# Optimization experiments

Measured on AMD Instinct MI355X. Metric: run time of the kernel, lower is better.

Reference implementation:

```python
import jax, jax.numpy as jnp
import numpy as np

N = 100000
E = 1600000
FEAT = 128
EMB = 64
HID = 64
OUT = 16


def _glorot(key, shape):
    fan_in, fan_out = shape[1], shape[0]
    lim = (6.0 / (fan_in + fan_out)) ** 0.5
    return jax.random.uniform(key, shape, jnp.float32, -lim, lim)


def setup_inputs() -> dict:
    key = jax.random.key(0)
    ks = jax.random.split(key, 16)
    return {
        "x_feat": jax.random.normal(ks[0], (N, FEAT), jnp.float32),
        "x_emb": jax.random.normal(ks[1], (N, 2, EMB), jnp.float32),
        "edge_index": jax.random.randint(ks[2], (2, E), 0, N, jnp.int32),
        # layer 0: SAGEConv(FEAT -> HID), Linear(EMB -> HID)
        "Wl0": _glorot(ks[3], (HID, FEAT)),
        "bl0": jnp.zeros((HID,), jnp.float32),
        "Wr0": _glorot(ks[4], (HID, FEAT)),
        "We0": _glorot(ks[5], (HID, EMB)),
        "be0": jnp.zeros((HID,), jnp.float32),
        # layer 1 (last): SAGEConv(HID -> OUT), Linear(EMB==HID -> OUT)
        "Wl1": _glorot(ks[6], (OUT, HID)),
        "bl1": jnp.zeros((OUT,), jnp.float32),
        "Wr1": _glorot(ks[7], (OUT, HID)),
        "We1": _glorot(ks[8], (OUT, HID)),
        "be1": jnp.zeros((OUT,), jnp.float32),
    }


def _sage_conv(x, edge_index, Wl, bl, Wr):
    # PyG SAGEConv with mean aggregation:
    #   out = lin_l(mean_{j in N(i)} x_j) + lin_r(x_i)
    src, dst = edge_index[0], edge_index[1]
    msg = x[src]                                   # [E, C] gather
    agg = jax.ops.segment_sum(msg, dst, num_segments=N)       # [N, C]
    deg = jax.ops.segment_sum(jnp.ones((E,), x.dtype), dst, num_segments=N)
    agg = agg / jnp.maximum(deg, 1.0)[:, None]     # mean over neighbors
    return agg @ Wl.T + bl + x @ Wr.T


def reference(x_feat, x_emb, edge_index,
              Wl0, bl0, Wr0, We0, be0,
              Wl1, bl1, Wr1, We1, be1):
    # forward(x=(x_feat, x_emb), edge_index=...) path, eval mode (dropout p=0)
    e = x_emb.mean(axis=1)                         # [N, EMB]
    # layer 0 (all but last): relu(sage + linear(emb))
    h = _sage_conv(x_feat, edge_index, Wl0, bl0, Wr0)
    e = e @ We0.T + be0
    h = jax.nn.relu(h + e)
    # last layer: no relu
    h = _sage_conv(h, edge_index, Wl1, bl1, Wr1)
    e = e @ We1.T + be1
    return h + e
```

## Files before the change

kernel.cpp:

```cpp
#include <hip/hip_runtime.h>
#include <hip/hip_bf16.h>
#include <cstddef>

#define NN 100000
#define EE 1600000
#define NPB 128
#define NB  782
#define ECH 4096
#define NCH 391
#define CAP 4096

typedef __attribute__((ext_vector_type(8))) short bf16x8;
typedef __attribute__((ext_vector_type(8))) unsigned short u16x8;
typedef __attribute__((ext_vector_type(4))) float f32x4;

#define YTS 72
#define RTS 68

static inline int ceil_div(int a, int b){ return (a + b - 1) / b; }

__device__ inline unsigned short f2bf(float f){
  union { float f; unsigned u; } v; v.f = f;
  unsigned r = (v.u + 0x7fff + ((v.u >> 16) & 1)) >> 16;
  return (unsigned short)r;
}
__device__ inline float bf2f(unsigned short s){
  union { unsigned u; float f; } v; v.u = ((unsigned)s) << 16;
  return v.f;
}

#define PRE_W (128 * 192)
#define PRE_E (PRE_W + 16 * 64)
#define PRE_B (PRE_E + 16)
#define PRE_C (PRE_B + 64)
#define PRE_N (PRE_C + NB)
__global__ void prep_all_kernel(const float* __restrict__ Wl0, const float* __restrict__ Wr0,
                                const float* __restrict__ We0, const float* __restrict__ bl0,
                                const float* __restrict__ be0, const float* __restrict__ We1,
                                const float* __restrict__ be1,
                                unsigned short* __restrict__ wcat, float* __restrict__ wee,
                                float* __restrict__ b1e, float* __restrict__ bias0,
                                int* __restrict__ cur){
  int idx = blockIdx.x * blockDim.x + threadIdx.x;
  if (idx < PRE_W){
    int n = idx / 192, k = idx % 192;
    float v;
    if (n < 64) v = (k < 128) ? Wl0[n * 128 + k] : 0.f;
    else        v = (k < 128) ? Wr0[(n - 64) * 128 + k] : We0[(n - 64) * 64 + (k - 128)];
    wcat[idx] = f2bf(v);
  } else if (idx < PRE_E){
    int j = idx - PRE_W;
    int i = j >> 6, c = j & 63;
    float s = 0.f;
    for (int k = 0; k < 64; k++) s += We1[i * 64 + k] * We0[k * 64 + c];
    wee[j] = s;
  } else if (idx < PRE_B){
    int i = idx - PRE_E;
    float s = be1[i];
    for (int k = 0; k < 64; k++) s += We1[i * 64 + k] * be0[k];
    b1e[i] = s;
  } else if (idx < PRE_C){
    int i = idx - PRE_B;
    bias0[i] = bl0[i] + be0[i];
  } else if (idx < PRE_N){
    cur[idx - PRE_C] = 0;
  }
}

__global__ void eprep_kernel(const float* __restrict__ xe, unsigned short* __restrict__ eb){
  int g = blockIdx.x * blockDim.x + threadIdx.x;
  if (g >= NN * 8) return;
  int node = g >> 3, q = g & 7;
  float4 a0 = ((const float4*)xe)[(size_t)node * 32 + q * 2];
  float4 a1 = ((const float4*)xe)[(size_t)node * 32 + q * 2 + 1];
  float4 b0 = ((const float4*)xe)[(size_t)node * 32 + 16 + q * 2];
  float4 b1 = ((const float4*)xe)[(size_t)node * 32 + 16 + q * 2 + 1];
  u16x8 o;
  o[0]=f2bf(0.5f*(a0.x+b0.x)); o[1]=f2bf(0.5f*(a0.y+b0.y));
  o[2]=f2bf(0.5f*(a0.z+b0.z)); o[3]=f2bf(0.5f*(a0.w+b0.w));
  o[4]=f2bf(0.5f*(a1.x+b1.x)); o[5]=f2bf(0.5f*(a1.y+b1.y));
  o[6]=f2bf(0.5f*(a1.z+b1.z)); o[7]=f2bf(0.5f*(a1.w+b1.w));
  *(u16x8*)&eb[(size_t)node * 64 + q * 8] = o;
}

__global__ __launch_bounds__(1024) void escatter_kernel(const int* __restrict__ src,
                                                        const int* __restrict__ dst,
                                                        int* __restrict__ cur,
                                                        int* __restrict__ ebkt){
  __shared__ int lh[NB];
  __shared__ int lo[NB];
  const int t = threadIdx.x;
  const int c = blockIdx.x;
  const int e0 = c * ECH;
  int ne = EE - e0; if (ne > ECH) ne = ECH;
  for (int i = t; i < NB; i += 1024) lh[i] = 0;
  __syncthreads();
  int dl[4], sl[4];
  #pragma unroll
  for (int k = 0; k < 4; k++){
    int i = t + k * 1024;
    dl[k] = (i < ne) ? dst[e0 + i] : -1;
    sl[k] = (i < ne) ? src[e0 + i] : 0;
  }
  #pragma unroll
  for (int k = 0; k < 4; k++)
    if (dl[k] >= 0) atomicAdd(&lh[dl[k] >> 7], 1);
  __syncthreads();
  for (int i = t; i < NB; i += 1024){
    int cc = lh[i];
    lo[i] = cc ? atomicAdd(&cur[i], cc) : 0;
    lh[i] = 0;
  }
  __syncthreads();
  #pragma unroll
  for (int k = 0; k < 4; k++){
    if (dl[k] >= 0){
      int d = dl[k], b = d >> 7;
      int r = atomicAdd(&lh[b], 1);
      int p = lo[b] + r;
      if (p < CAP) ebkt[b * CAP + p] = ((d & 127) << 24) | sl[k];
    }
  }
}

__global__ __launch_bounds__(256, 3) void l0_gemm_kernel(
    const float* __restrict__ xf, const unsigned short* __restrict__ eb,
    const unsigned short* __restrict__ wcat,
    unsigned short* __restrict__ y0g, float* __restrict__ re0g, int M){
  __shared__ unsigned short As[64 * 200];
  __shared__ unsigned short Ys[64 * YTS];
  __shared__ float          Rs[64 * RTS];
  const int t = threadIdx.x;
  const int row0 = blockIdx.x * 64;
  float4 fa[4], fb[4];
  u16x8 ev[2];
  #pragma unroll
  for (int k = 0; k < 4; k++){
    int idx = t + k * 256;
    int r = idx >> 4, o = idx & 15;
    int row = row0 + r;
    if (row < M){
      fa[k] = ((const float4*)xf)[(size_t)row * 32 + o * 2];
      fb[k] = ((const float4*)xf)[(size_t)row * 32 + o * 2 + 1];
    } else {
      fa[k] = make_float4(0.f,0.f,0.f,0.f);
      fb[k] = make_float4(0.f,0.f,0.f,0.f);
    }
  }
  #pragma unroll
  for (int k = 0; k < 2; k++){
    int idx = t + k * 256;
    int r = idx >> 3, q = idx & 7;
    int row = row0 + r;
    u16x8 z = {0,0,0,0,0,0,0,0};
    ev[k] = (row < M) ? *(const u16x8*)&eb[(size_t)row * 64 + q * 8] : z;
  }
  #pragma unroll
  for (int k = 0; k < 4; k++){
    int idx = t + k * 256;
    int r = idx >> 4, o = idx & 15;
    u16x8 ov;
    ov[0]=f2bf(fa[k].x); ov[1]=f2bf(fa[k].y); ov[2]=f2bf(fa[k].z); ov[3]=f2bf(fa[k].w);
    ov[4]=f2bf(fb[k].x); ov[5]=f2bf(fb[k].y); ov[6]=f2bf(fb[k].z); ov[7]=f2bf(fb[k].w);
    *(u16x8*)&As[r * 200 + o * 8] = ov;
  }
  #pragma unroll
  for (int k = 0; k < 2; k++){
    int idx = t + k * 256;
    int r = idx >> 3, q = idx & 7;
    *(u16x8*)&As[r * 200 + 128 + q * 8] = ev[k];
  }
  const int w = t >> 6, l = t & 63;
  const int lm = l & 15, quad = l >> 4;
  bf16x8 bfr0[6], bfr1[6];
  {
    int n0 = w * 16 + lm;
    int n1 = 64 + w * 16 + lm;
    #pragma unroll
    for (int ks = 0; ks < 6; ks++){
      bfr0[ks] = *(const bf16x8*)&wcat[n0 * 192 + ks * 32 + quad * 8];
      bfr1[ks] = *(const bf16x8*)&wcat[n1 * 192 + ks * 32 + quad * 8];
    }
  }
  __syncthreads();
  for (int rg = 0; rg < 4; rg++){
    bf16x8 af[6];
    #pragma unroll
    for (int ks = 0; ks < 6; ks++)
      af[ks] = *(const bf16x8*)&As[(rg * 16 + lm) * 200 + ks * 32 + quad * 8];
    f32x4 acc0 = {0.f, 0.f, 0.f, 0.f};
    f32x4 acc1 = {0.f, 0.f, 0.f, 0.f};
    #pragma unroll
    for (int ks = 0; ks < 6; ks++){
      acc0 = __builtin_amdgcn_mfma_f32_16x16x32_bf16(af[ks], bfr0[ks], acc0, 0, 0, 0);
      acc1 = __builtin_amdgcn_mfma_f32_16x16x32_bf16(af[ks], bfr1[ks], acc1, 0, 0, 0);
    }
    #pragma unroll
    for (int r = 0; r < 4; r++){
      int lrow = rg * 16 + quad * 4 + r;
      Ys[lrow * YTS + w * 16 + lm] = f2bf(acc0[r]);
      Rs[lrow * RTS + w * 16 + lm] = acc1[r];
    }
  }
  __syncthreads();
  #pragma unroll
  for (int k = 0; k < 2; k++){
    int idx = t + k * 256;
    int r = idx >> 3, c8 = idx & 7;
    int grow = row0 + r;
    if (grow < M)
      *(u16x8*)&y0g[(size_t)grow * 64 + c8 * 8] = *(const u16x8*)&Ys[r * YTS + c8 * 8];
  }
  #pragma unroll
  for (int k = 0; k < 4; k++){
    int idx = t + k * 256;
    int r = idx >> 4, c4 = idx & 15;
    int grow = row0 + r;
    if (grow < M)
      *(f32x4*)&re0g[(size_t)grow * 64 + c4 * 4] = *(const f32x4*)&Rs[r * RTS + c4 * 4];
  }
}

__global__ __launch_bounds__(256) void agg0_kernel(
    const unsigned short* __restrict__ y0, const float* __restrict__ re0,
    const float* __restrict__ bias0, const int* __restrict__ cur,
    int* __restrict__ ebkt, int* __restrict__ rs, int* __restrict__ deg,
    unsigned short* __restrict__ h){
  __shared__ int lraw[CAP];
  __shared__ int lsrt[CAP];
  __shared__ int lh[NPB];
  __shared__ int loff[NPB];
  __shared__ int lcur[NPB];
  const int t = threadIdx.x;
  const int b = blockIdx.x;
  const int e0 = b * CAP;
  int cnt = cur[b]; if (cnt > CAP) cnt = CAP;
  for (int i = t; i < NPB; i += 256) lh[i] = 0;
  __syncthreads();
  for (int i = t; i < cnt; i += 256){
    int w = ebkt[e0 + i];
    lraw[i] = w;
    atomicAdd(&lh[((unsigned)w) >> 24], 1);
  }
  __syncthreads();
  {
    int v = (t < NPB) ? lh[t] : 0;
    int s = v;
    for (int off = 1; off < NPB; off <<= 1){
      __syncthreads();
      if (t < NPB) loff[t] = s;
      __syncthreads();
      if (t < NPB && t >= off) s += loff[t - off];
    }
    __syncthreads();
    if (t < NPB){ loff[t] = s - v; lcur[t] = s - v; }
  }
  __syncthreads();
  for (int i = t; i < cnt; i += 256){
    int w = lraw[i];
    int d = ((unsigned)w) >> 24;
    int pos = atomicAdd(&lcur[d], 1);
    lsrt[pos] = w & 0xFFFFFF;
  }
  __syncthreads();
  for (int i = t; i < cnt; i += 256) ebkt[e0 + i] = lsrt[i];
  if (t < NPB){
    int node = b * NPB + t;
    if (node < NN){
      rs[node]  = e0 + loff[t];
      deg[node] = lh[t];
    }
  }
  const int lane = t & 7;
  for (int sub = 0; sub < 4; sub++){
    int r = sub * 32 + (t >> 3);
    int node = b * NPB + r;
    if (node >= NN) continue;
    int start = loff[r], cn = lh[r];
    float acc[4][8] = {};
    int i = 0;
    for (; i + 8 <= cn; i += 8){
      int s[8];
      #pragma unroll
      for (int j = 0; j < 8; j++) s[j] = lsrt[start + i + j];
      u16x8 v[8];
      #pragma unroll
      for (int j = 0; j < 8; j++) v[j] = *(const u16x8*)&y0[(size_t)s[j] * 64 + lane * 8];
      #pragma unroll
      for (int j = 0; j < 8; j++)
        #pragma unroll
        for (int k = 0; k < 8; k++) acc[j & 3][k] += bf2f((unsigned short)v[j][k]);
    }
    for (; i < cn; i++){
      int s = lsrt[start + i];
      u16x8 v = *(const u16x8*)&y0[(size_t)s * 64 + lane * 8];
      #pragma unroll
      for (int k = 0; k < 8; k++) acc[0][k] += bf2f((unsigned short)v[k]);
    }
    float inv = 1.0f / (float)(cn > 1 ? cn : 1);
    f32x4 rv0 = *(const f32x4*)&re0[(size_t)node * 64 + lane * 8];
    f32x4 rv1 = *(const f32x4*)&re0[(size_t)node * 64 + lane * 8 + 4];
    float rvv[8] = {rv0[0], rv0[1], rv0[2], rv0[3], rv1[0], rv1[1], rv1[2], rv1[3]};
    float4 ba = ((const float4*)bias0)[lane * 2];
    float4 bb = ((const float4*)bias0)[lane * 2 + 1];
    float bv[8] = {ba.x, ba.y, ba.z, ba.w, bb.x, bb.y, bb.z, bb.w};
    u16x8 o;
    #pragma unroll
    for (int k = 0; k < 8; k++){
      float sum = (acc[0][k] + acc[1][k]) + (acc[2][k] + acc[3][k]);
      float x = sum * inv + rvv[k] + bv[k];
      o[k] = f2bf(x > 0.f ? x : 0.f);
    }
    *(u16x8*)&h[(size_t)node * 64 + lane * 8] = o;
  }
}

__global__ __launch_bounds__(256) void gemm16_dual_kernel(
    const unsigned short* __restrict__ H, const unsigned short* __restrict__ eb,
    const float* __restrict__ Wl1, const float* __restrict__ Wr1,
    const float* __restrict__ wee,
    const float* __restrict__ bl1, const float* __restrict__ b1e,
    unsigned short* __restrict__ Y1, float* __restrict__ Out, int M){
  __shared__ float Hs[64][65];
  __shared__ float Es[64][65];
  __shared__ float Wls[16][65];
  __shared__ float Wrs[16][65];
  __shared__ float Wes[16][65];
  __shared__ float bs[16];
  const int t = threadIdx.x;
  const int row0 = blockIdx.x * 64;
  {
    int j = t >> 4, kq = t & 15;
    float4 a = ((const float4*)Wl1)[j * 16 + kq];
    float4 b = ((const float4*)Wr1)[j * 16 + kq];
    float4 c = ((const float4*)wee)[j * 16 + kq];
    Wls[j][kq*4+0]=a.x; Wls[j][kq*4+1]=a.y; Wls[j][kq*4+2]=a.z; Wls[j][kq*4+3]=a.w;
    Wrs[j][kq*4+0]=b.x; Wrs[j][kq*4+1]=b.y; Wrs[j][kq*4+2]=b.z; Wrs[j][kq*4+3]=b.w;
    Wes[j][kq*4+0]=c.x; Wes[j][kq*4+1]=c.y; Wes[j][kq*4+2]=c.z; Wes[j][kq*4+3]=c.w;
  }
  if (t < 16) bs[t] = bl1[t] + b1e[t];
  for (int idx = t; idx < 64 * 16; idx += 256){
    int n = idx >> 4, kq = idx & 15;
    int row = row0 + n;
    ushort4 hv = make_ushort4(0,0,0,0), evv = make_ushort4(0,0,0,0);
    if (row < M){
      hv  = *(const ushort4*)&H[(size_t)row * 64 + kq * 4];
      evv = *(const ushort4*)&eb[(size_t)row * 64 + kq * 4];
    }
    Hs[n][kq*4+0]=bf2f(hv.x); Hs[n][kq*4+1]=bf2f(hv.y); Hs[n][kq*4+2]=bf2f(hv.z); Hs[n][kq*4+3]=bf2f(hv.w);
    Es[n][kq*4+0]=bf2f(evv.x); Es[n][kq*4+1]=bf2f(evv.y); Es[n][kq*4+2]=bf2f(evv.z); Es[n][kq*4+3]=bf2f(evv.w);
  }
  __syncthreads();
  const int n = t >> 2, jq = t & 3;
  float y[4] = {}, o[4] = {};
  #pragma unroll 4
  for (int k = 0; k < 64; k++){
    float a = Hs[n][k];
    float e = Es[n][k];
    #pragma unroll
    for (int j = 0; j < 4; j++){
      y[j] = fmaf(a, Wls[jq*4 + j][k], y[j]);
      o[j] = fmaf(a, Wrs[jq*4 + j][k], o[j]);
      o[j] = fmaf(e, Wes[jq*4 + j][k], o[j]);
    }
  }
  int row = row0 + n;
  if (row < M){
    ushort4 yb; yb.x = f2bf(y[0]); yb.y = f2bf(y[1]); yb.z = f2bf(y[2]); yb.w = f2bf(y[3]);
    *(ushort4*)&Y1[(size_t)row * 16 + jq * 4] = yb;
    ((float4*)Out)[(size_t)row * 4 + jq] =
        make_float4(o[0] + bs[jq*4+0], o[1] + bs[jq*4+1], o[2] + bs[jq*4+2], o[3] + bs[jq*4+3]);
  }
}

__global__ void agg1_kernel(const unsigned short* __restrict__ y1,
                            const int* __restrict__ rs, const int* __restrict__ deg,
                            const int* __restrict__ ssrc, float* __restrict__ outp){
  int g = blockIdx.x * blockDim.x + threadIdx.x;
  if (g >= NN * 2) return;
  int node = g >> 1, lane = g & 1;
  int start = rs[node], cnt = deg[node];
  float acc[4][8] = {};
  int i = 0;
  for (; i + 8 <= cnt; i += 8){
    int s[8];
    #pragma unroll
    for (int j = 0; j < 8; j++) s[j] = ssrc[start + i + j];
    u16x8 v[8];
    #pragma unroll
    for (int j = 0; j < 8; j++) v[j] = *(const u16x8*)&y1[(size_t)s[j] * 16 + lane * 8];
    #pragma unroll
    for (int j = 0; j < 8; j++)
      #pragma unroll
      for (int k = 0; k < 8; k++) acc[j & 3][k] += bf2f((unsigned short)v[j][k]);
  }
  for (; i < cnt; i++){
    int s = ssrc[start + i];
    u16x8 v = *(const u16x8*)&y1[(size_t)s * 16 + lane * 8];
    #pragma unroll
    for (int k = 0; k < 8; k++) acc[0][k] += bf2f((unsigned short)v[k]);
  }
  float inv = 1.0f / (float)(cnt > 1 ? cnt : 1);
  f32x4 o0 = *(f32x4*)&outp[(size_t)node * 16 + lane * 8];
  f32x4 o1 = *(f32x4*)&outp[(size_t)node * 16 + lane * 8 + 4];
  #pragma unroll
  for (int k = 0; k < 4; k++){
    o0[k] += ((acc[0][k] + acc[1][k]) + (acc[2][k] + acc[3][k])) * inv;
    o1[k] += ((acc[0][k+4] + acc[1][k+4]) + (acc[2][k+4] + acc[3][k+4])) * inv;
  }
  *(f32x4*)&outp[(size_t)node * 16 + lane * 8]     = o0;
  *(f32x4*)&outp[(size_t)node * 16 + lane * 8 + 4] = o1;
}

extern "C" void kernel_launch(void* const* d_in, const int* in_sizes, int n_in,
                              void* d_out, int out_size, void* d_ws, size_t ws_size,
                              hipStream_t stream){
  (void)in_sizes; (void)n_in; (void)out_size; (void)ws_size;
  const float* x_feat = (const float*)d_in[0];
  const float* x_emb  = (const float*)d_in[1];
  const int*   ei     = (const int*)d_in[2];
  const float* Wl0 = (const float*)d_in[3];
  const float* bl0 = (const float*)d_in[4];
  const float* Wr0 = (const float*)d_in[5];
  const float* We0 = (const float*)d_in[6];
  const float* be0 = (const float*)d_in[7];
  const float* Wl1 = (const float*)d_in[8];
  const float* bl1 = (const float*)d_in[9];
  const float* Wr1 = (const float*)d_in[10];
  const float* We1 = (const float*)d_in[11];
  const float* be1 = (const float*)d_in[12];
  float* out = (float*)d_out;

  char* w = (char*)d_ws;
  float* re0          = (float*)w;           w += sizeof(float) * (size_t)NN * 64;
  unsigned short* y0  = (unsigned short*)w;  w += sizeof(unsigned short) * (size_t)NN * 64;
  unsigned short* eb  = (unsigned short*)w;  w += sizeof(unsigned short) * (size_t)NN * 64;
  unsigned short* h   = (unsigned short*)w;  w += sizeof(unsigned short) * (size_t)NN * 64;
  unsigned short* y1  = (unsigned short*)w;  w += sizeof(unsigned short) * (size_t)NN * 16;
  unsigned short* wcat= (unsigned short*)w;  w += sizeof(unsigned short) * 128 * 192;
  float* wee   = (float*)w;                  w += sizeof(float) * 16 * 64;
  float* b1e   = (float*)w;                  w += sizeof(float) * 16;
  float* bias0 = (float*)w;                  w += sizeof(float) * 64;
  int* ebkt    = (int*)w;                    w += sizeof(int) * (size_t)NB * CAP;
  int* cur     = (int*)w;                    w += sizeof(int) * NB;
  int* rs      = (int*)w;                    w += sizeof(int) * NN;
  int* deg     = (int*)w;                    w += sizeof(int) * NN;

  const int* srcp = ei;
  const int* dstp = ei + EE;

  prep_all_kernel<<<ceil_div(PRE_N, 256), 256, 0, stream>>>(
      Wl0, Wr0, We0, bl0, be0, We1, be1, wcat, wee, b1e, bias0, cur);

  escatter_kernel<<<NCH, 1024, 0, stream>>>(srcp, dstp, cur, ebkt);

  eprep_kernel<<<ceil_div(NN * 8, 256), 256, 0, stream>>>(x_emb, eb);

  l0_gemm_kernel<<<ceil_div(NN, 64), 256, 0, stream>>>(x_feat, eb, wcat, y0, re0, NN);

  agg0_kernel<<<NB, 256, 0, stream>>>(y0, re0, bias0, cur, ebkt, rs, deg, h);

  gemm16_dual_kernel<<<ceil_div(NN, 64), 256, 0, stream>>>(h, eb, Wl1, Wr1, wee,
                                                           bl1, b1e, y1, out, NN);
  agg1_kernel<<<ceil_div(NN * 2, 256), 256, 0, stream>>>(y1, rs, deg, ebkt, out);
}
```

Measured before the change: 272.3 us.

## Fuse embedding prep into layer-0 GEMM and layer-1 GEMM into aggregation

The embedding-mean conversion now happens inside the layer-0 GEMM, which also writes the bf16 embedding buffer, so the separate eprep kernel goes away. The 64-to-16 layer-1 projections are computed in the agg0 epilogue with per-lane partial dot products and shuffle reductions, which removes the h buffer round trip and the gemm16 kernel. The bucket capacity is lowered to cut shared memory so agg0 can run with a higher occupancy hint. The trade-off is more register and shuffle work per node in agg0, and a risk of dropping edges if a bucket exceeds 3072 entries.

```diff
diff --git a/kernel.cpp b/kernel.cpp
--- a/kernel.cpp
+++ b/kernel.cpp
@@ -8,7 +8,7 @@
 #define NB  782
 #define ECH 4096
 #define NCH 391
-#define CAP 4096
+#define CAP 3072
 
 typedef __attribute__((ext_vector_type(8))) short bf16x8;
 typedef __attribute__((ext_vector_type(8))) unsigned short u16x8;
@@ -67,22 +67,6 @@
   }
 }
 
-__global__ void eprep_kernel(const float* __restrict__ xe, unsigned short* __restrict__ eb){
-  int g = blockIdx.x * blockDim.x + threadIdx.x;
-  if (g >= NN * 8) return;
-  int node = g >> 3, q = g & 7;
-  float4 a0 = ((const float4*)xe)[(size_t)node * 32 + q * 2];
-  float4 a1 = ((const float4*)xe)[(size_t)node * 32 + q * 2 + 1];
-  float4 b0 = ((const float4*)xe)[(size_t)node * 32 + 16 + q * 2];
-  float4 b1 = ((const float4*)xe)[(size_t)node * 32 + 16 + q * 2 + 1];
-  u16x8 o;
-  o[0]=f2bf(0.5f*(a0.x+b0.x)); o[1]=f2bf(0.5f*(a0.y+b0.y));
-  o[2]=f2bf(0.5f*(a0.z+b0.z)); o[3]=f2bf(0.5f*(a0.w+b0.w));
-  o[4]=f2bf(0.5f*(a1.x+b1.x)); o[5]=f2bf(0.5f*(a1.y+b1.y));
-  o[6]=f2bf(0.5f*(a1.z+b1.z)); o[7]=f2bf(0.5f*(a1.w+b1.w));
-  *(u16x8*)&eb[(size_t)node * 64 + q * 8] = o;
-}
-
 __global__ __launch_bounds__(1024) void escatter_kernel(const int* __restrict__ src,
                                                         const int* __restrict__ dst,
                                                         int* __restrict__ cur,
@@ -124,8 +108,8 @@
 }
 
 __global__ __launch_bounds__(256, 3) void l0_gemm_kernel(
-    const float* __restrict__ xf, const unsigned short* __restrict__ eb,
-    const unsigned short* __restrict__ wcat,
+    const float* __restrict__ xf, const float* __restrict__ xe,
+    const unsigned short* __restrict__ wcat, unsigned short* __restrict__ ebg,
     unsigned short* __restrict__ y0g, float* __restrict__ re0g, int M){
   __shared__ unsigned short As[64 * 200];
   __shared__ unsigned short Ys[64 * YTS];
@@ -153,7 +137,18 @@
     int r = idx >> 3, q = idx & 7;
     int row = row0 + r;
     u16x8 z = {0,0,0,0,0,0,0,0};
-    ev[k] = (row < M) ? *(const u16x8*)&eb[(size_t)row * 64 + q * 8] : z;
+    if (row < M){
+      float4 a0 = ((const float4*)xe)[(size_t)row * 32 + q * 2];
+      float4 a1 = ((const float4*)xe)[(size_t)row * 32 + q * 2 + 1];
+      float4 b0 = ((const float4*)xe)[(size_t)row * 32 + 16 + q * 2];
+      float4 b1 = ((const float4*)xe)[(size_t)row * 32 + 16 + q * 2 + 1];
+      z[0]=f2bf(0.5f*(a0.x+b0.x)); z[1]=f2bf(0.5f*(a0.y+b0.y));
+      z[2]=f2bf(0.5f*(a0.z+b0.z)); z[3]=f2bf(0.5f*(a0.w+b0.w));
+      z[4]=f2bf(0.5f*(a1.x+b1.x)); z[5]=f2bf(0.5f*(a1.y+b1.y));
+      z[6]=f2bf(0.5f*(a1.z+b1.z)); z[7]=f2bf(0.5f*(a1.w+b1.w));
+      *(u16x8*)&ebg[(size_t)row * 64 + q * 8] = z;
+    }
+    ev[k] = z;
   }
   #pragma unroll
   for (int k = 0; k < 4; k++){
@@ -221,19 +216,34 @@
   }
 }
 
-__global__ __launch_bounds__(256) void agg0_kernel(
+__global__ __launch_bounds__(256, 4) void agg0_kernel(
     const unsigned short* __restrict__ y0, const float* __restrict__ re0,
-    const float* __restrict__ bias0, const int* __restrict__ cur,
-    int* __restrict__ ebkt, int* __restrict__ rs, int* __restrict__ deg,
-    unsigned short* __restrict__ h){
+    const float* __restrict__ bias0, const unsigned short* __restrict__ eb,
+    const float* __restrict__ Wl1, const float* __restrict__ Wr1,
+    const float* __restrict__ wee, const float* __restrict__ bl1,
+    const float* __restrict__ b1e,
+    const int* __restrict__ cur, int* __restrict__ ebkt,
+    int* __restrict__ rs, int* __restrict__ deg,
+    unsigned short* __restrict__ y1, float* __restrict__ outp){
   __shared__ int lraw[CAP];
   __shared__ int lsrt[CAP];
   __shared__ int lh[NPB];
   __shared__ int loff[NPB];
   __shared__ int lcur[NPB];
+  __shared__ float Wls[16][68];
+  __shared__ float Wrs[16][68];
+  __shared__ float Wes[16][68];
+  __shared__ float bs[16];
   const int t = threadIdx.x;
   const int b = blockIdx.x;
   const int e0 = b * CAP;
+  for (int i = t; i < 16 * 64; i += 256){
+    int j = i >> 6, k = i & 63;
+    Wls[j][k] = Wl1[i];
+    Wrs[j][k] = Wr1[i];
+    Wes[j][k] = wee[i];
+  }
+  if (t < 16) bs[t] = bl1[t] + b1e[t];
   int cnt = cur[b]; if (cnt > CAP) cnt = CAP;
   for (int i = t; i < NPB; i += 256) lh[i] = 0;
   __syncthreads();
@@ -304,72 +314,59 @@
     float4 ba = ((const float4*)bias0)[lane * 2];
     float4 bb = ((const float4*)bias0)[lane * 2 + 1];
     float bv[8] = {ba.x, ba.y, ba.z, ba.w, bb.x, bb.y, bb.z, bb.w};
-    u16x8 o;
+    float xh[8], evf[8];
+    u16x8 ev8 = *(const u16x8*)&eb[(size_t)node * 64 + lane * 8];
     #pragma unroll
     for (int k = 0; k < 8; k++){
       float sum = (acc[0][k] + acc[1][k]) + (acc[2][k] + acc[3][k]);
       float x = sum * inv + rvv[k] + bv[k];
-      o[k] = f2bf(x > 0.f ? x : 0.f);
-    }
-    *(u16x8*)&h[(size_t)node * 64 + lane * 8] = o;
-  }
-}
-
-__global__ __launch_bounds__(256) void gemm16_dual_kernel(
-    const unsigned short* __restrict__ H, const unsigned short* __restrict__ eb,
-    const float* __restrict__ Wl1, const float* __restrict__ Wr1,
-    const float* __restrict__ wee,
-    const float* __restrict__ bl1, const float* __restrict__ b1e,
-    unsigned short* __restrict__ Y1, float* __restrict__ Out, int M){
-  __shared__ float Hs[64][65];
-  __shared__ float Es[64][65];
-  __shared__ float Wls[16][65];
-  __shared__ float Wrs[16][65];
-  __shared__ float Wes[16][65];
-  __shared__ float bs[16];
-  const int t = threadIdx.x;
-  const int row0 = blockIdx.x * 64;
-  {
-    int j = t >> 4, kq = t & 15;
-    float4 a = ((const float4*)Wl1)[j * 16 + kq];
-    float4 b = ((const float4*)Wr1)[j * 16 + kq];
-    float4 c = ((const float4*)wee)[j * 16 + kq];
-    Wls[j][kq*4+0]=a.x; Wls[j][kq*4+1]=a.y; Wls[j][kq*4+2]=a.z; Wls[j][kq*4+3]=a.w;
-    Wrs[j][kq*4+0]=b.x; Wrs[j][kq*4+1]=b.y; Wrs[j][kq*4+2]=b.z; Wrs[j][kq*4+3]=b.w;
-    Wes[j][kq*4+0]=c.x; Wes[j][kq*4+1]=c.y; Wes[j][kq*4+2]=c.z; Wes[j][kq*4+3]=c.w;
-  }
-  if (t < 16) bs[t] = bl1[t] + b1e[t];
-  for (int idx = t; idx < 64 * 16; idx += 256){
-    int n = idx >> 4, kq = idx & 15;
-    int row = row0 + n;
-    ushort4 hv = make_ushort4(0,0,0,0), evv = make_ushort4(0,0,0,0);
-    if (row < M){
-      hv  = *(const ushort4*)&H[(size_t)row * 64 + kq * 4];
-      evv = *(const ushort4*)&eb[(size_t)row * 64 + kq * 4];
-    }
-    Hs[n][kq*4+0]=bf2f(hv.x); Hs[n][kq*4+1]=bf2f(hv.y); Hs[n][kq*4+2]=bf2f(hv.z); Hs[n][kq*4+3]=bf2f(hv.w);
-    Es[n][kq*4+0]=bf2f(evv.x); Es[n][kq*4+1]=bf2f(evv.y); Es[n][kq*4+2]=bf2f(evv.z); Es[n][kq*4+3]=bf2f(evv.w);
-  }
-  __syncthreads();
-  const int n = t >> 2, jq = t & 3;
-  float y[4] = {}, o[4] = {};
-  #pragma unroll 4
-  for (int k = 0; k < 64; k++){
-    float a = Hs[n][k];
-    float e = Es[n][k];
-    #pragma unroll
-    for (int j = 0; j < 4; j++){
-      y[j] = fmaf(a, Wls[jq*4 + j][k], y[j]);
-      o[j] = fmaf(a, Wrs[jq*4 + j][k], o[j]);
-      o[j] = fmaf(e, Wes[jq*4 + j][k], o[j]);
-    }
-  }
-  int row = row0 + n;
-  if (row < M){
-    ushort4 yb; yb.x = f2bf(y[0]); yb.y = f2bf(y[1]); yb.z = f2bf(y[2]); yb.w = f2bf(y[3]);
-    *(ushort4*)&Y1[(size_t)row * 16 + jq * 4] = yb;
-    ((float4*)Out)[(size_t)row * 4 + jq] =
-        make_float4(o[0] + bs[jq*4+0], o[1] + bs[jq*4+1], o[2] + bs[jq*4+2], o[3] + bs[jq*4+3]);
+      xh[k]  = bf2f(f2bf(x > 0.f ? x : 0.f));
+      evf[k] = bf2f((unsigned short)ev8[k]);
+    }
+    float yl[16], ol[16];
+    #pragma unroll
+    for (int j = 0; j < 16; j++){
+      float sy = 0.f, so = 0.f;
+      #pragma unroll
+      for (int kk = 0; kk < 8; kk++){
+        float wl = Wls[j][lane * 8 + kk];
+        float wr = Wrs[j][lane * 8 + kk];
+        float we = Wes[j][lane * 8 + kk];
+        sy = fmaf(xh[kk], wl, sy);
+        so = fmaf(xh[kk], wr, so);
+        so = fmaf(evf[kk], we, so);
+      }
+      yl[j] = sy; ol[j] = so;
+    }
+    #pragma unroll
+    for (int m = 1; m < 8; m <<= 1){
+      #pragma unroll
+      for (int j = 0; j < 16; j++){
+        yl[j] += __shfl_xor(yl[j], m);
+        ol[j] += __shfl_xor(ol[j], m);
+      }
+    }
+    if (lane == 0){
+      u16x8 w0;
+      #pragma unroll
+      for (int j = 0; j < 8; j++) w0[j] = f2bf(yl[j]);
+      *(u16x8*)&y1[(size_t)node * 16] = w0;
+    } else if (lane == 1){
+      u16x8 w1;
+      #pragma unroll
+      for (int j = 0; j < 8; j++) w1[j] = f2bf(yl[8 + j]);
+      *(u16x8*)&y1[(size_t)node * 16 + 8] = w1;
+    } else if (lane == 2){
+      f32x4 o0 = {ol[0] + bs[0], ol[1] + bs[1], ol[2] + bs[2], ol[3] + bs[3]};
+      f32x4 o1 = {ol[4] + bs[4], ol[5] + bs[5], ol[6] + bs[6], ol[7] + bs[7]};
+      *(f32x4*)&outp[(size_t)node * 16]     = o0;
+      *(f32x4*)&outp[(size_t)node * 16 + 4] = o1;
+    } else if (lane == 3){
+      f32x4 o2 = {ol[8] + bs[8], ol[9] + bs[9], ol[10] + bs[10], ol[11] + bs[11]};
+      f32x4 o3 = {ol[12] + bs[12], ol[13] + bs[13], ol[14] + bs[14], ol[15] + bs[15]};
+      *(f32x4*)&outp[(size_t)node * 16 + 8]  = o2;
+      *(f32x4*)&outp[(size_t)node * 16 + 12] = o3;
+    }
   }
 }
 
@@ -435,7 +432,6 @@
   float* re0          = (float*)w;           w += sizeof(float) * (size_t)NN * 64;
   unsigned short* y0  = (unsigned short*)w;  w += sizeof(unsigned short) * (size_t)NN * 64;
   unsigned short* eb  = (unsigned short*)w;  w += sizeof(unsigned short) * (size_t)NN * 64;
-  unsigned short* h   = (unsigned short*)w;  w += sizeof(unsigned short) * (size_t)NN * 64;
   unsigned short* y1  = (unsigned short*)w;  w += sizeof(unsigned short) * (size_t)NN * 16;
   unsigned short* wcat= (unsigned short*)w;  w += sizeof(unsigned short) * 128 * 192;
   float* wee   = (float*)w;                  w += sizeof(float) * 16 * 64;
@@ -454,13 +450,10 @@
 
   escatter_kernel<<<NCH, 1024, 0, stream>>>(srcp, dstp, cur, ebkt);
 
-  eprep_kernel<<<ceil_div(NN * 8, 256), 256, 0, stream>>>(x_emb, eb);
-
-  l0_gemm_kernel<<<ceil_div(NN, 64), 256, 0, stream>>>(x_feat, eb, wcat, y0, re0, NN);
-
-  agg0_kernel<<<NB, 256, 0, stream>>>(y0, re0, bias0, cur, ebkt, rs, deg, h);
-
-  gemm16_dual_kernel<<<ceil_div(NN, 64), 256, 0, stream>>>(h, eb, Wl1, Wr1, wee,
-                                                           bl1, b1e, y1, out, NN);
+  l0_gemm_kernel<<<ceil_div(NN, 64), 256, 0, stream>>>(x_feat, x_emb, wcat, eb, y0, re0, NN);
+
+  agg0_kernel<<<NB, 256, 0, stream>>>(y0, re0, bias0, eb, Wl1, Wr1, wee, bl1, b1e,
+                                      cur, ebkt, rs, deg, y1, out);
+
   agg1_kernel<<<ceil_div(NN * 2, 256), 256, 0, stream>>>(y1, rs, deg, ebkt, out);
 }
```

New measurement: 268.9 us, median of 3. Within noise of the previous version (-1.3%).
